# Kernel tuning notes

Measured on AMD Instinct MI355X. Metric: run time of the kernel, lower is better.

Reference implementation:

```python
import jax, jax.numpy as jnp
import numpy as np

LEAKY_SLOPE = 0.2
N_HEADS = 8
INPUT_DIM = 128
HEAD_DIM = 16  # embed_dim=128 // n_heads=8


def setup_inputs() -> dict:
    key = jax.random.key(0)
    k1, k2, k3, k4 = jax.random.split(key, 4)
    b, n = 4, 512
    h = jax.random.normal(k1, (b, n, INPUT_DIM), dtype=jnp.float32)
    mask = jnp.zeros((b, n, n), dtype=bool)  # 1 = attention not possible
    stdv_w = 1.0 / np.sqrt(HEAD_DIM)
    Wl = jax.random.uniform(k2, (N_HEADS, INPUT_DIM, HEAD_DIM), minval=-stdv_w, maxval=stdv_w, dtype=jnp.float32)
    Wr = jax.random.uniform(k3, (N_HEADS, INPUT_DIM, HEAD_DIM), minval=-stdv_w, maxval=stdv_w, dtype=jnp.float32)
    # Wak in torch is (n_heads, head_dim, 1); stdv = 1/sqrt(size(-1)) = 1
    Wak = jax.random.uniform(k4, (N_HEADS, HEAD_DIM), minval=-1.0, maxval=1.0, dtype=jnp.float32)
    return {"h": h, "mask": mask, "Wl": Wl, "Wr": Wr, "Wak": Wak}


def reference(h, mask, Wl, Wr, Wak):
    b, n, _ = h.shape
    # per-head projections: g = h @ W  -> (heads, batch, N, head_dim)
    g_l = jnp.einsum('bni,hid->hbnd', h, Wl)
    g_r = jnp.einsum('bni,hid->hbnd', h, Wr)
    # additive attention: LeakyReLU(g_l_i + g_r_j) . a  -> (heads, batch, N, N)
    e = jax.nn.leaky_relu(g_l[:, :, :, None, :] + g_r[:, :, None, :, :],
                          negative_slope=LEAKY_SLOPE)
    scores = jnp.einsum('hbijd,hd->hbij', e, Wak)
    scores = jnp.where(mask[None], -jnp.inf, scores)
    attn = jax.nn.softmax(scores, axis=-1)
    # weighted sum of g_r, then ReLU; output layout (batch, N, heads*head_dim)
    h_prime = jax.nn.relu(jnp.einsum('hbij,hbjd->bihd', attn, g_r))
    return h_prime.reshape(b, n, -1)
```

## Files before the change

### kernel.cpp

```cpp
#include <hip/hip_runtime.h>
#include <hip/hip_bf16.h>

#define B_SZ 4
#define N_SZ 512
#define IN_DIM 128
#define NH 8
#define HD 16
#define SLOPE 0.2f

#define ROWS 64
#define JT   8
#define JSEG 2
#define JB   (N_SZ / JSEG)
#define TPB  512
#define GR_STRIDE 20
#define GLS_STRIDE 20

typedef float v2f __attribute__((ext_vector_type(2)));

#define WS_GL 0
#define WS_GR (NH * B_SZ * N_SZ * HD)
#define WS_OP (2 * WS_GR)
#define WS_LP (WS_OP + NH * B_SZ * JSEG * N_SZ * HD)
#define WS_TOT (WS_LP + NH * B_SZ * JSEG * N_SZ)

__global__ __launch_bounds__(256) void proj_kernel(
    const float* __restrict__ hin, const float* __restrict__ Wl,
    const float* __restrict__ Wr, float* __restrict__ gl, float* __restrict__ gr)
{
    int row = blockIdx.x;
    __shared__ float hrow[IN_DIM];
    int t = threadIdx.x;
    if (t < IN_DIM) hrow[t] = hin[(size_t)row * IN_DIM + t];
    __syncthreads();

    int side = t >> 7;
    int hd = t & 127;
    int head = hd >> 4, d = hd & 15;
    const float* W = (side ? Wr : Wl) + head * (IN_DIM * HD) + d;
    float acc = 0.f;
#pragma unroll 16
    for (int k = 0; k < IN_DIM; ++k)
        acc = fmaf(hrow[k], W[k * HD], acc);

    int b = row >> 9, i = row & (N_SZ - 1);
    float* g = side ? gr : gl;
    g[((size_t)(head * B_SZ + b) * N_SZ + i) * HD + d] = acc;
}

__global__ __launch_bounds__(TPB, 4) void attn_part_kernel(
    const float* __restrict__ gl, const float* __restrict__ gr,
    const float* __restrict__ Wak, const unsigned char* __restrict__ mask,
    float* __restrict__ opart, float* __restrict__ lpart)
{
    __shared__ float grs[JB * GR_STRIDE];
    __shared__ float gls[ROWS * GLS_STRIDE];
    __shared__ float crs[JB];

    int bid = blockIdx.x;
    int seg = bid & (JSEG - 1);
    int itile = (bid >> 1) & 7;
    int hb = bid >> 4;
    int head = hb >> 2, b = hb & 3;
    int t = threadIdx.x;
    int j0 = seg * JB;

    int il = t >> 3;
    int jt = t & 7;
    int i = itile * ROWS + il;

    const float* grp = gr + ((size_t)hb * N_SZ + j0) * HD;
    for (int idx4 = t; idx4 < JB * HD / 4; idx4 += TPB) {
        float4 v = ((const float4*)grp)[idx4];
        int j = idx4 >> 2, dq = (idx4 & 3) * 4;
        float* p = &grs[j * GR_STRIDE + dq];
        *(v2f*)p = (v2f){v.x, v.y};
        *(v2f*)(p + 2) = (v2f){v.z, v.w};
    }
    const float* glp = gl + ((size_t)hb * N_SZ + itile * ROWS) * HD;
#pragma unroll
    for (int k = 0; k < 2; ++k) {
        int idx = k * TPB + t;
        gls[(idx >> 4) * GLS_STRIDE + (idx & 15)] = glp[idx];
    }

    const unsigned char* mrow = mask + ((size_t)(b * N_SZ + i)) * N_SZ + j0;
    unsigned mbits = 0;
#pragma unroll
    for (int jj = 0; jj < JB / JT; ++jj)
        mbits |= (mrow[jj * JT + jt] ? 1u : 0u) << jj;

    __syncthreads();

    const float* ap = Wak + head * HD;

    if (t < JB) {
        const float* r = &grs[t * GR_STRIDE];
        float acc = 0.f;
#pragma unroll
        for (int dd = 0; dd < HD; ++dd) acc = fmaf(ap[dd], r[dd], acc);
        crs[t] = 0.6f * acc;
    }

    v2f glv[HD / 2], o[HD / 2];
    const float* grow = &gls[il * GLS_STRIDE];
#pragma unroll
    for (int e = 0; e < HD / 2; ++e) glv[e] = *(const v2f*)(grow + 2 * e);
    float cl06;
    {
        float acc = 0.f;
#pragma unroll
        for (int dd = 0; dd < HD; ++dd) acc = fmaf(ap[dd], grow[dd], acc);
        cl06 = 0.6f * acc;
    }
#pragma unroll
    for (int e = 0; e < HD / 2; ++e) o[e] = (v2f){0.f, 0.f};

    __syncthreads();

    float l = 0.f;

#pragma unroll 2
    for (int jj = 0; jj < JB / JT; ++jj) {
        int j = jj * JT + jt;
        const float* r = &grs[j * GR_STRIDE];
        float4 g01 = *(const float4*)(r);
        float4 g23 = *(const float4*)(r + 4);
        float4 g45 = *(const float4*)(r + 8);
        float4 g67 = *(const float4*)(r + 12);
        v2f gj[HD / 2] = {
            (v2f){g01.x, g01.y}, (v2f){g01.z, g01.w},
            (v2f){g23.x, g23.y}, (v2f){g23.z, g23.w},
            (v2f){g45.x, g45.y}, (v2f){g45.z, g45.w},
            (v2f){g67.x, g67.y}, (v2f){g67.z, g67.w}};

        float s0 = 0.f, s1 = 0.f;
#pragma unroll
        for (int e = 0; e < HD / 2; ++e) {
            v2f x = glv[e] + gj[e];
            s0 = fmaf(ap[2 * e],     fabsf(x.x), s0);
            s1 = fmaf(ap[2 * e + 1], fabsf(x.y), s1);
        }
        float s = fmaf(0.4f, s0 + s1, cl06 + crs[j]);
        s = fminf(s, 80.f);
        if (mbits & (1u << jj)) s = -1e30f;

        float p = __expf(s);
        l += p;
        v2f pv = (v2f){p, p};
#pragma unroll
        for (int e = 0; e < HD / 2; ++e)
            o[e] += pv * gj[e];
    }

#pragma unroll
    for (int off = 1; off < JT; off <<= 1) {
        l += __shfl_xor(l, off, 64);
#pragma unroll
        for (int e = 0; e < HD / 2; ++e) {
            v2f other;
            other.x = __shfl_xor(o[e].x, off, 64);
            other.y = __shfl_xor(o[e].y, off, 64);
            o[e] += other;
        }
    }

    if (jt == 0) {
        float res[HD];
#pragma unroll
        for (int e = 0; e < HD / 2; ++e) { res[2 * e] = o[e].x; res[2 * e + 1] = o[e].y; }
        float* op = opart + ((size_t)(hb * JSEG + seg) * N_SZ + i) * HD;
        *(float4*)op = *(float4*)res;
        *(float4*)(op + 4) = *(float4*)(res + 4);
        *(float4*)(op + 8) = *(float4*)(res + 8);
        *(float4*)(op + 12) = *(float4*)(res + 12);
        lpart[(size_t)(hb * JSEG + seg) * N_SZ + i] = l;
    }
}

__global__ __launch_bounds__(256) void combine_kernel(
    const float* __restrict__ opart, const float* __restrict__ lpart,
    float* __restrict__ out)
{
    int gid = blockIdx.x * 256 + threadIdx.x;
    int d = gid & 15;
    int r = gid >> 4;
    int i = r & (N_SZ - 1);
    int hb = r >> 9;
    int head = hb >> 2, b = hb & 3;

    float o = opart[((size_t)(hb * JSEG + 0) * N_SZ + i) * HD + d]
            + opart[((size_t)(hb * JSEG + 1) * N_SZ + i) * HD + d];
    float l = lpart[(size_t)(hb * JSEG + 0) * N_SZ + i]
            + lpart[(size_t)(hb * JSEG + 1) * N_SZ + i];
    out[((size_t)(b * N_SZ + i)) * (NH * HD) + head * HD + d] = fmaxf(o / l, 0.f);
}

__global__ __launch_bounds__(TPB) void gatv2_fused(
    const float* __restrict__ hin, const unsigned char* __restrict__ mask,
    const float* __restrict__ Wl, const float* __restrict__ Wr,
    const float* __restrict__ Wak, float* __restrict__ out)
{
    __shared__ float wrs[IN_DIM * HD];
    __shared__ float hsh[32][IN_DIM + 1];
    __shared__ float grs[N_SZ * 18];
    __shared__ float gls[32][HD];

    int bid = blockIdx.x;
    int itile = bid & 15;
    int hb = bid >> 4;
    int head = hb >> 2, b = hb & 3;
    int t = threadIdx.x;

    int jl = t >> 4;
    int d  = t & 15;

    for (int idx = t; idx < IN_DIM * HD; idx += TPB)
        wrs[idx] = Wr[head * IN_DIM * HD + idx];

    const float* hb_base = hin + (size_t)b * N_SZ * IN_DIM;
    const float* wlcol = Wl + head * IN_DIM * HD + d;

    for (int c = 0; c < N_SZ / 32; ++c) {
        __syncthreads();
        const float* hc = hb_base + (size_t)c * 32 * IN_DIM;
        for (int idx = t; idx < 32 * IN_DIM; idx += TPB)
            hsh[idx >> 7][idx & 127] = hc[idx];
        __syncthreads();

        float acc = 0.f;
#pragma unroll 16
        for (int k = 0; k < IN_DIM; ++k)
            acc = fmaf(hsh[jl][k], wrs[k * HD + d], acc);
        grs[(c * 32 + jl) * 18 + d] = acc;

        if (c == itile) {
            float accl = 0.f;
#pragma unroll 16
            for (int k = 0; k < IN_DIM; ++k)
                accl = fmaf(hsh[jl][k], wlcol[k * HD], accl);
            gls[jl][d] = accl;
        }
    }
    __syncthreads();

    int il = jl;
    int jt = d;
    int i = itile * 32 + il;

    float glv[HD], avv[HD];
#pragma unroll
    for (int dd = 0; dd < HD; ++dd) glv[dd] = gls[il][dd];
    const float* ap = Wak + head * HD;
#pragma unroll
    for (int dd = 0; dd < HD; ++dd) avv[dd] = ap[dd];

    const unsigned char* mrow = mask + ((size_t)(b * N_SZ + i)) * N_SZ;

    float m = -1e30f, l = 0.f;
    float o[HD];
#pragma unroll
    for (int dd = 0; dd < HD; ++dd) o[dd] = 0.f;

    for (int jj = 0; jj < N_SZ / 16; ++jj) {
        int j = jj * 16 + jt;
        const float* r = &grs[j * 18];
        float gj[HD];
#pragma unroll
        for (int e = 0; e < HD / 2; ++e) {
            float2 v = *(const float2*)(r + 2 * e);
            gj[2 * e] = v.x; gj[2 * e + 1] = v.y;
        }

        float s = 0.f;
#pragma unroll
        for (int dd = 0; dd < HD; ++dd) {
            float x = glv[dd] + gj[dd];
            float lr = fmaxf(x, SLOPE * x);
            s = fmaf(avv[dd], lr, s);
        }
        if (mrow[j]) s = -1e30f;

        float mn = fmaxf(m, s);
        float cc = __expf(m - mn);
        float p = __expf(s - mn);
        l = fmaf(l, cc, p);
#pragma unroll
        for (int dd = 0; dd < HD; ++dd)
            o[dd] = fmaf(o[dd], cc, p * gj[dd]);
        m = mn;
    }

#pragma unroll
    for (int off = 1; off < 16; off <<= 1) {
        float mo = __shfl_xor(m, off, 64);
        float lo = __shfl_xor(l, off, 64);
        float mn = fmaxf(m, mo);
        float c1 = __expf(m - mn), c2 = __expf(mo - mn);
        l = l * c1 + lo * c2;
#pragma unroll
        for (int dd = 0; dd < HD; ++dd)
            o[dd] = o[dd] * c1 + __shfl_xor(o[dd], off, 64) * c2;
        m = mn;
    }

    if (jt == 0) {
        float inv = 1.f / l;
        float res[HD];
#pragma unroll
        for (int dd = 0; dd < HD; ++dd)
            res[dd] = fmaxf(o[dd] * inv, 0.f);
        float* op = out + ((size_t)(b * N_SZ + i)) * (NH * HD) + head * HD;
#pragma unroll
        for (int e = 0; e < HD / 4; ++e)
            *(float4*)(op + 4 * e) = *(float4*)(res + 4 * e);
    }
}

extern "C" void kernel_launch(void* const* d_in, const int* in_sizes, int n_in,
                              void* d_out, int out_size, void* d_ws, size_t ws_size,
                              hipStream_t stream) {
    const float* hin = (const float*)d_in[0];
    const unsigned char* mask = (const unsigned char*)d_in[1];
    const float* Wl = (const float*)d_in[2];
    const float* Wr = (const float*)d_in[3];
    const float* Wak = (const float*)d_in[4];
    float* out = (float*)d_out;
    (void)in_sizes; (void)n_in; (void)out_size;

    const size_t need = (size_t)WS_TOT * sizeof(float);

    if (ws_size >= need && d_ws != nullptr) {
        float* ws = (float*)d_ws;
        float* gl = ws + WS_GL;
        float* gr = ws + WS_GR;
        float* op = ws + WS_OP;
        float* lp = ws + WS_LP;
        proj_kernel<<<B_SZ * N_SZ, 256, 0, stream>>>(hin, Wl, Wr, gl, gr);
        attn_part_kernel<<<NH * B_SZ * (N_SZ / ROWS) * JSEG, TPB, 0, stream>>>(
            gl, gr, Wak, mask, op, lp);
        combine_kernel<<<(NH * B_SZ * N_SZ * HD) / 256, 256, 0, stream>>>(
            op, lp, out);
    } else {
        gatv2_fused<<<NH * B_SZ * (N_SZ / 32), TPB, 0, stream>>>(
            hin, mask, Wl, Wr, Wak, out);
    }
}
```

Baseline: 94.89 us.

## Replace projection with tiled GEMM and drop split-J attention plus combine kernel

Result: faster. 86.52 us (-8.8%).

```diff
diff --git a/kernel.cpp b/kernel.cpp
--- a/kernel.cpp
+++ b/kernel.cpp
@@ -8,10 +8,8 @@
 #define HD 16
 #define SLOPE 0.2f
 
-#define ROWS 64
-#define JT   8
-#define JSEG 2
-#define JB   (N_SZ / JSEG)
+#define ROWS 32
+#define JT   16
 #define TPB  512
 #define GR_STRIDE 20
 #define GLS_STRIDE 20
@@ -20,81 +18,127 @@
 
 #define WS_GL 0
 #define WS_GR (NH * B_SZ * N_SZ * HD)
-#define WS_OP (2 * WS_GR)
-#define WS_LP (WS_OP + NH * B_SZ * JSEG * N_SZ * HD)
-#define WS_TOT (WS_LP + NH * B_SZ * JSEG * N_SZ)
-
-__global__ __launch_bounds__(256) void proj_kernel(
+#define WS_TOT (2 * WS_GR)
+
+#define PM 32
+#define PKC 64
+#define AT_S 38
+#define BT_S 68
+
+__global__ __launch_bounds__(256) void proj_gemm(
     const float* __restrict__ hin, const float* __restrict__ Wl,
     const float* __restrict__ Wr, float* __restrict__ gl, float* __restrict__ gr)
 {
-    int row = blockIdx.x;
-    __shared__ float hrow[IN_DIM];
+    __shared__ float At[PKC * AT_S];
+    __shared__ float Bs[PKC * BT_S];
+
+    int rt = blockIdx.x >> 2;
+    int ct = blockIdx.x & 3;
+    int side = ct >> 1;
+    int headbase = (ct & 1) * 4;
+    const float* Wsrc = side ? Wr : Wl;
+    int rowbase = rt * PM;
+
     int t = threadIdx.x;
-    if (t < IN_DIM) hrow[t] = hin[(size_t)row * IN_DIM + t];
-    __syncthreads();
-
-    int side = t >> 7;
-    int hd = t & 127;
-    int head = hd >> 4, d = hd & 15;
-    const float* W = (side ? Wr : Wl) + head * (IN_DIM * HD) + d;
-    float acc = 0.f;
+    int ty = t >> 4;
+    int tx = t & 15;
+
+    float acc[2][4] = {{0.f,0.f,0.f,0.f},{0.f,0.f,0.f,0.f}};
+
+    for (int kc = 0; kc < IN_DIM; kc += PKC) {
+        __syncthreads();
+#pragma unroll
+        for (int it = 0; it < 2; ++it) {
+            int task = it * 256 + t;
+            int r = task >> 4, kq = task & 15;
+            float4 v = *(const float4*)&hin[(size_t)(rowbase + r) * IN_DIM + kc + kq * 4];
+            At[(kq * 4 + 0) * AT_S + r] = v.x;
+            At[(kq * 4 + 1) * AT_S + r] = v.y;
+            At[(kq * 4 + 2) * AT_S + r] = v.z;
+            At[(kq * 4 + 3) * AT_S + r] = v.w;
+        }
+#pragma unroll
+        for (int it = 0; it < 4; ++it) {
+            int task = it * 256 + t;
+            int k = task >> 4, cc4 = task & 15;
+            int head = headbase + (cc4 >> 2);
+            int dq = (cc4 & 3) * 4;
+            float4 v = *(const float4*)&Wsrc[head * (IN_DIM * HD) + (kc + k) * HD + dq];
+            *(float4*)&Bs[k * BT_S + cc4 * 4] = v;
+        }
+        __syncthreads();
+
 #pragma unroll 16
-    for (int k = 0; k < IN_DIM; ++k)
-        acc = fmaf(hrow[k], W[k * HD], acc);
-
-    int b = row >> 9, i = row & (N_SZ - 1);
+        for (int k = 0; k < PKC; ++k) {
+            float2 a = *(const float2*)&At[k * AT_S + ty * 2];
+            float4 b = *(const float4*)&Bs[k * BT_S + tx * 4];
+            acc[0][0] = fmaf(a.x, b.x, acc[0][0]);
+            acc[0][1] = fmaf(a.x, b.y, acc[0][1]);
+            acc[0][2] = fmaf(a.x, b.z, acc[0][2]);
+            acc[0][3] = fmaf(a.x, b.w, acc[0][3]);
+            acc[1][0] = fmaf(a.y, b.x, acc[1][0]);
+            acc[1][1] = fmaf(a.y, b.y, acc[1][1]);
+            acc[1][2] = fmaf(a.y, b.z, acc[1][2]);
+            acc[1][3] = fmaf(a.y, b.w, acc[1][3]);
+        }
+    }
+
+    int head = headbase + (tx >> 2);
+    int d4 = (tx & 3) * 4;
     float* g = side ? gr : gl;
-    g[((size_t)(head * B_SZ + b) * N_SZ + i) * HD + d] = acc;
+#pragma unroll
+    for (int r = 0; r < 2; ++r) {
+        int row = rowbase + ty * 2 + r;
+        int b = row >> 9, i = row & (N_SZ - 1);
+        float4 v = {acc[r][0], acc[r][1], acc[r][2], acc[r][3]};
+        *(float4*)&g[((size_t)(head * B_SZ + b) * N_SZ + i) * HD + d4] = v;
+    }
 }
 
-__global__ __launch_bounds__(TPB, 4) void attn_part_kernel(
+__global__ __launch_bounds__(TPB, 4) void attn_kernel(
     const float* __restrict__ gl, const float* __restrict__ gr,
     const float* __restrict__ Wak, const unsigned char* __restrict__ mask,
-    float* __restrict__ opart, float* __restrict__ lpart)
+    float* __restrict__ out)
 {
-    __shared__ float grs[JB * GR_STRIDE];
+    __shared__ float grs[N_SZ * GR_STRIDE];
     __shared__ float gls[ROWS * GLS_STRIDE];
-    __shared__ float crs[JB];
+    __shared__ float crs[N_SZ];
 
     int bid = blockIdx.x;
-    int seg = bid & (JSEG - 1);
-    int itile = (bid >> 1) & 7;
+    int itile = bid & 15;
     int hb = bid >> 4;
     int head = hb >> 2, b = hb & 3;
     int t = threadIdx.x;
-    int j0 = seg * JB;
-
-    int il = t >> 3;
-    int jt = t & 7;
+
+    int il = t >> 4;
+    int jt = t & 15;
     int i = itile * ROWS + il;
 
-    const float* grp = gr + ((size_t)hb * N_SZ + j0) * HD;
-    for (int idx4 = t; idx4 < JB * HD / 4; idx4 += TPB) {
+    const float* grp = gr + (size_t)hb * (N_SZ * HD);
+#pragma unroll
+    for (int it = 0; it < 4; ++it) {
+        int idx4 = it * TPB + t;
         float4 v = ((const float4*)grp)[idx4];
         int j = idx4 >> 2, dq = (idx4 & 3) * 4;
-        float* p = &grs[j * GR_STRIDE + dq];
-        *(v2f*)p = (v2f){v.x, v.y};
-        *(v2f*)(p + 2) = (v2f){v.z, v.w};
+        *(float4*)&grs[j * GR_STRIDE + dq] = v;
     }
     const float* glp = gl + ((size_t)hb * N_SZ + itile * ROWS) * HD;
-#pragma unroll
-    for (int k = 0; k < 2; ++k) {
-        int idx = k * TPB + t;
-        gls[(idx >> 4) * GLS_STRIDE + (idx & 15)] = glp[idx];
-    }
-
-    const unsigned char* mrow = mask + ((size_t)(b * N_SZ + i)) * N_SZ + j0;
+    {
+        int row = t >> 4, d = t & 15;
+        gls[row * GLS_STRIDE + d] = glp[t];
+    }
+
+    const unsigned char* mrow = mask + ((size_t)(b * N_SZ + i)) * N_SZ;
     unsigned mbits = 0;
 #pragma unroll
-    for (int jj = 0; jj < JB / JT; ++jj)
+    for (int jj = 0; jj < N_SZ / JT; ++jj)
         mbits |= (mrow[jj * JT + jt] ? 1u : 0u) << jj;
 
     __syncthreads();
 
     const float* ap = Wak + head * HD;
 
-    if (t < JB) {
+    {
         const float* r = &grs[t * GR_STRIDE];
         float acc = 0.f;
 #pragma unroll
@@ -121,7 +165,7 @@
     float l = 0.f;
 
 #pragma unroll 2
-    for (int jj = 0; jj < JB / JT; ++jj) {
+    for (int jj = 0; jj < N_SZ / JT; ++jj) {
         int j = jj * JT + jt;
         const float* r = &grs[j * GR_STRIDE];
         float4 g01 = *(const float4*)(r);
@@ -166,34 +210,19 @@
     }
 
     if (jt == 0) {
+        float inv = 1.f / l;
         float res[HD];
 #pragma unroll
-        for (int e = 0; e < HD / 2; ++e) { res[2 * e] = o[e].x; res[2 * e + 1] = o[e].y; }
-        float* op = opart + ((size_t)(hb * JSEG + seg) * N_SZ + i) * HD;
+        for (int e = 0; e < HD / 2; ++e) {
+            res[2 * e]     = fmaxf(o[e].x * inv, 0.f);
+            res[2 * e + 1] = fmaxf(o[e].y * inv, 0.f);
+        }
+        float* op = out + ((size_t)(b * N_SZ + i)) * (NH * HD) + head * HD;
         *(float4*)op = *(float4*)res;
         *(float4*)(op + 4) = *(float4*)(res + 4);
         *(float4*)(op + 8) = *(float4*)(res + 8);
         *(float4*)(op + 12) = *(float4*)(res + 12);
-        lpart[(size_t)(hb * JSEG + seg) * N_SZ + i] = l;
-    }
-}
-
-__global__ __launch_bounds__(256) void combine_kernel(
-    const float* __restrict__ opart, const float* __restrict__ lpart,
-    float* __restrict__ out)
-{
-    int gid = blockIdx.x * 256 + threadIdx.x;
-    int d = gid & 15;
-    int r = gid >> 4;
-    int i = r & (N_SZ - 1);
-    int hb = r >> 9;
-    int head = hb >> 2, b = hb & 3;
-
-    float o = opart[((size_t)(hb * JSEG + 0) * N_SZ + i) * HD + d]
-            + opart[((size_t)(hb * JSEG + 1) * N_SZ + i) * HD + d];
-    float l = lpart[(size_t)(hb * JSEG + 0) * N_SZ + i]
-            + lpart[(size_t)(hb * JSEG + 1) * N_SZ + i];
-    out[((size_t)(b * N_SZ + i)) * (NH * HD) + head * HD + d] = fmaxf(o / l, 0.f);
+    }
 }
 
 __global__ __launch_bounds__(TPB) void gatv2_fused(
@@ -244,8 +273,7 @@
     }
     __syncthreads();
 
-    int il = jl;
-    int jt = d;
+    int il = jl, jt = d;
     int i = itile * 32 + il;
 
     float glv[HD], avv[HD];
@@ -334,13 +362,9 @@
         float* ws = (float*)d_ws;
         float* gl = ws + WS_GL;
         float* gr = ws + WS_GR;
-        float* op = ws + WS_OP;
-        float* lp = ws + WS_LP;
-        proj_kernel<<<B_SZ * N_SZ, 256, 0, stream>>>(hin, Wl, Wr, gl, gr);
-        attn_part_kernel<<<NH * B_SZ * (N_SZ / ROWS) * JSEG, TPB, 0, stream>>>(
-            gl, gr, Wak, mask, op, lp);
-        combine_kernel<<<(NH * B_SZ * N_SZ * HD) / 256, 256, 0, stream>>>(
-            op, lp, out);
+        proj_gemm<<<(B_SZ * N_SZ / PM) * 4, 256, 0, stream>>>(hin, Wl, Wr, gl, gr);
+        attn_kernel<<<NH * B_SZ * (N_SZ / ROWS), TPB, 0, stream>>>(
+            gl, gr, Wak, mask, out);
     } else {
         gatv2_fused<<<NH * B_SZ * (N_SZ / 32), TPB, 0, stream>>>(
             hin, mask, Wl, Wr, Wak, out);
```
